# Kernel tuning notes

Hardware: AMD Instinct MI355X
Metric: run time of the kernel (lower is better)

## Reference

```python
import jax, jax.numpy as jnp
import numpy as np

# Static config (matches init_kwargs)
H, G, D = 16, 4, 128          # n_head, n_query_groups, head_size
QPK = H // G                  # queries per kv group = 4
LEFT = 1024 - 1               # sliding-window left width (local_window-1)
SCALE = 1.0 / float(np.sqrt(D))
NEG = jnp.finfo(jnp.float32).min


def _rope(x, cos, sin):
    # x: [B,T,h,D]; cos/sin: [T, D/2]; non-interleaved (flash-attn) convention
    d2 = cos.shape[-1]
    x1, x2 = x[..., :d2], x[..., d2:]
    c = cos[None, :, None, :]
    s = sin[None, :, None, :]
    return jnp.concatenate([x1 * c - x2 * s, x1 * s + x2 * c], axis=-1)


def setup_inputs() -> dict:
    key = jax.random.key(0)
    ks = jax.random.split(key, 4)
    B, T, C = 1, 2048, 2048
    x = jax.random.normal(ks[0], (B, T, C), jnp.float32)
    # real RoPE tables, base 10000
    pos = jnp.arange(T, dtype=jnp.float32)
    inv_freq = 1.0 / (10000.0 ** (jnp.arange(0, D, 2, dtype=jnp.float32) / D))
    ang = pos[:, None] * inv_freq[None, :]        # [T, D/2]
    cos, sin = jnp.cos(ang), jnp.sin(ang)
    W_attn = jax.random.normal(ks[1], ((H + 2 * G) * D, C), jnp.float32) * 0.02
    W_proj = jax.random.normal(ks[2], (C, H * D), jnp.float32) * 0.02
    k_sink = jax.random.normal(ks[3], (G * D,), jnp.float32) * 0.02
    v_sink = jnp.zeros((G * D,), jnp.float32)     # buffer, zeros in original
    return {"x": x, "cos": cos, "sin": sin, "W_attn": W_attn,
            "W_proj": W_proj, "k_sink": k_sink, "v_sink": v_sink}


def reference(x, cos, sin, W_attn, W_proj, k_sink, v_sink):
    B, T, C = x.shape
    # fused QKV projection (no bias)
    qkv = jnp.einsum('btc,oc->bto', x, W_attn)                 # [B,T,(H+2G)*D]
    qkv = qkv.reshape(B, T, G, QPK + 2, D)
    q = qkv[:, :, :, :QPK, :].reshape(B, T, H, D)              # [B,T,H,D]
    k = qkv[:, :, :, QPK, :]                                   # [B,T,G,D]
    v = qkv[:, :, :, QPK + 1, :]                               # [B,T,G,D]
    # RoPE on q and k
    q = _rope(q, cos, sin)
    k = _rope(k, cos, sin)
    # prepend sink token to k/v -> seqlen_k = T+1
    k = jnp.concatenate([jnp.broadcast_to(k_sink.reshape(1, 1, G, D), (B, 1, G, D)), k], axis=1)
    v = jnp.concatenate([jnp.broadcast_to(v_sink.reshape(1, 1, G, D), (B, 1, G, D)), v], axis=1)
    Tk = T + 1
    # GQA: group-major query head layout -> head h uses kv group h // QPK
    kh = jnp.repeat(k, QPK, axis=2)                            # [B,Tk,H,D]
    vh = jnp.repeat(v, QPK, axis=2)
    scores = jnp.einsum('bqhd,bkhd->bhqk', q, kh) * SCALE      # [B,H,T,Tk]
    # flash-attn causal + sliding window, bottom-right aligned: offset = Tk - T
    off = Tk - T
    i = jnp.arange(T)[:, None]
    j = jnp.arange(Tk)[None, :]
    allowed = (j <= i + off) & (j >= i + off - LEFT)
    scores = jnp.where(allowed[None, None], scores, NEG)
    p = jax.nn.softmax(scores, axis=-1)
    o = jnp.einsum('bhqk,bkhd->bqhd', p, vh).reshape(B, T, H * D)
    y = jnp.einsum('btd,cd->btc', o, W_proj)                   # output proj, no bias
    return y
```

## Files before the change

### kernel.cpp

```cpp
#include <hip/hip_runtime.h>

#define T_SEQ  2048
#define TK_SEQ 2049
#define JP     2080
#define SCALE_F 0.08838834764831845f
#define SL_F    0.12751744f
#define THR_L2  11.0f

typedef __attribute__((ext_vector_type(8))) short short8;
typedef __attribute__((ext_vector_type(4))) float f32x4;

__device__ __forceinline__ unsigned short f2bf(float f) {
  unsigned int u = __float_as_uint(f);
  u += 0x7fff + ((u >> 16) & 1);
  return (unsigned short)(u >> 16);
}

__global__ __launch_bounds__(256) void split_pack(const float4* __restrict__ s0,
                                                  uint4* __restrict__ d0, int n0,
                                                  const float4* __restrict__ s1,
                                                  uint4* __restrict__ d1, int n1) {
  int i = blockIdx.x * 256 + threadIdx.x;
  const float4* s; uint4* d; int k;
  if (i < n0) { s = s0; d = d0; k = i; }
  else { k = i - n0; if (k >= n1) return; s = s1; d = d1; }
  float4 f = s[k];
  unsigned int h0 = __float_as_uint(f.x) & 0xffff0000u;
  unsigned int h1 = __float_as_uint(f.y) & 0xffff0000u;
  unsigned int h2 = __float_as_uint(f.z) & 0xffff0000u;
  unsigned int h3 = __float_as_uint(f.w) & 0xffff0000u;
  unsigned int l0 = f2bf(f.x - __uint_as_float(h0));
  unsigned int l1 = f2bf(f.y - __uint_as_float(h1));
  unsigned int l2 = f2bf(f.z - __uint_as_float(h2));
  unsigned int l3 = f2bf(f.w - __uint_as_float(h3));
  uint4 o;
  o.x = (h0 >> 16) | (h1 & 0xffff0000u);
  o.y = (h2 >> 16) | (h3 & 0xffff0000u);
  o.z = l0 | (l1 << 16);
  o.w = l2 | (l3 << 16);
  d[k] = o;
}

#define LDK 56

__global__ __launch_bounds__(256, 3) void gemm_sp(const uint4* __restrict__ As,
                                                  const uint4* __restrict__ Bs,
                                                  float* __restrict__ C,
                                                  int M, int N, int K) {
  __shared__ unsigned short Ah[128 * LDK], Al[128 * LDK];
  __shared__ unsigned short Bh[64 * LDK],  Bl[64 * LDK];

  const int tid  = threadIdx.x;
  const int lane = tid & 63;
  const int wid  = tid >> 6;
  const int wm   = (wid >> 1) << 6;
  const int wn   = (wid & 1) << 5;
  const int lo16 = lane & 15;
  const int hi4  = lane >> 4;
  const int m0   = blockIdx.y << 7;
  const int n0   = blockIdx.x << 6;
  const int Kg   = K >> 2;

  const uint4* pa[4];
  const uint4* pb[2];
  int waofs[4], wbofs[2];
#pragma unroll
  for (int v = 0; v < 4; ++v) {
    int id = (v << 8) + tid;
    int r  = id >> 3;
    int kc = (id & 7) << 2;
    pa[v]    = As + (size_t)(m0 + r) * Kg + (kc >> 2);
    waofs[v] = r * LDK + kc;
  }
#pragma unroll
  for (int v = 0; v < 2; ++v) {
    int id = (v << 8) + tid;
    int r  = id >> 3;
    int kc = (id & 7) << 2;
    pb[v]    = Bs + (size_t)(n0 + r) * Kg + (kc >> 2);
    wbofs[v] = r * LDK + kc;
  }

  int ra[4], rb[2];
#pragma unroll
  for (int i = 0; i < 4; ++i) ra[i] = (wm + i * 16 + lo16) * LDK + (hi4 << 3);
#pragma unroll
  for (int j = 0; j < 2; ++j) rb[j] = (wn + j * 16 + lo16) * LDK + (hi4 << 3);

  f32x4 acc[4][2];
  const f32x4 z4 = {0.f, 0.f, 0.f, 0.f};
#pragma unroll
  for (int i = 0; i < 4; ++i)
#pragma unroll
    for (int j = 0; j < 2; ++j) acc[i][j] = z4;

  uint4 av[4], bv[2];
#pragma unroll
  for (int v = 0; v < 4; ++v) av[v] = pa[v][0];
#pragma unroll
  for (int v = 0; v < 2; ++v) bv[v] = pb[v][0];

  for (int k0 = 0; k0 < K; k0 += 32) {
    __syncthreads();
#pragma unroll
    for (int v = 0; v < 4; ++v) {
      uint2 ah = {av[v].x, av[v].y}, al = {av[v].z, av[v].w};
      *(uint2*)&Ah[waofs[v]] = ah;
      *(uint2*)&Al[waofs[v]] = al;
    }
#pragma unroll
    for (int v = 0; v < 2; ++v) {
      uint2 bh = {bv[v].x, bv[v].y}, bl = {bv[v].z, bv[v].w};
      *(uint2*)&Bh[wbofs[v]] = bh;
      *(uint2*)&Bl[wbofs[v]] = bl;
    }
    __syncthreads();
    if (k0 + 32 < K) {
      int kg = (k0 + 32) >> 2;
#pragma unroll
      for (int v = 0; v < 4; ++v) av[v] = pa[v][kg];
#pragma unroll
      for (int v = 0; v < 2; ++v) bv[v] = pb[v][kg];
    }
    short8 fah[4], fal[4], fbh[2], fbl[2];
#pragma unroll
    for (int i = 0; i < 4; ++i) {
      fah[i] = *(const short8*)&Ah[ra[i]];
      fal[i] = *(const short8*)&Al[ra[i]];
    }
#pragma unroll
    for (int j = 0; j < 2; ++j) {
      fbh[j] = *(const short8*)&Bh[rb[j]];
      fbl[j] = *(const short8*)&Bl[rb[j]];
    }
#pragma unroll
    for (int i = 0; i < 4; ++i)
#pragma unroll
      for (int j = 0; j < 2; ++j) {
        acc[i][j] = __builtin_amdgcn_mfma_f32_16x16x32_bf16(fah[i], fbh[j], acc[i][j], 0, 0, 0);
        acc[i][j] = __builtin_amdgcn_mfma_f32_16x16x32_bf16(fal[i], fbh[j], acc[i][j], 0, 0, 0);
        acc[i][j] = __builtin_amdgcn_mfma_f32_16x16x32_bf16(fah[i], fbl[j], acc[i][j], 0, 0, 0);
      }
  }

#pragma unroll
  for (int i = 0; i < 4; ++i) {
    const int row = m0 + wm + i * 16 + (hi4 << 2);
#pragma unroll
    for (int j = 0; j < 2; ++j) {
      float* cp = C + (size_t)row * N + n0 + wn + j * 16 + lo16;
      cp[0]            = acc[i][j][0];
      cp[(size_t)N]    = acc[i][j][1];
      cp[(size_t)2*N]  = acc[i][j][2];
      cp[(size_t)3*N]  = acc[i][j][3];
    }
  }
}

#define RB_Q  4096
#define RB_K  1024
#define RB_KE 64
#define RB_V  65

__global__ __launch_bounds__(256) void rope2(const float* __restrict__ qkv,
                                             const float* __restrict__ cosb,
                                             const float* __restrict__ sinb,
                                             const float* __restrict__ ksink,
                                             const float* __restrict__ vsink,
                                             unsigned short* __restrict__ qb,
                                             unsigned short* __restrict__ kb,
                                             unsigned short* __restrict__ vtb) {
  __shared__ unsigned short tl[512 * 33];
  const int bid = blockIdx.x, tid = threadIdx.x;
  if (bid < RB_Q) {
    int idx = bid * 256 + tid;
    int t = idx >> 9, rem = idx & 511;
    int h = rem >> 5, dp = (rem & 31) << 1;
    int g = h >> 2, qi = h & 3;
    const float* src = qkv + (size_t)t * 3072 + g * 768 + qi * 128;
    float2 x1 = *(const float2*)(src + dp);
    float2 x2 = *(const float2*)(src + 64 + dp);
    float2 c  = *(const float2*)(cosb + t * 64 + dp);
    float2 s  = *(const float2*)(sinb + t * 64 + dp);
    ushort2 o1 = { f2bf(x1.x * c.x - x2.x * s.x), f2bf(x1.y * c.y - x2.y * s.y) };
    ushort2 o2 = { f2bf(x1.x * s.x + x2.x * c.x), f2bf(x1.y * s.y + x2.y * c.y) };
    *(ushort2*)(qb + (size_t)t * 2048 + h * 128 + dp)      = o1;
    *(ushort2*)(qb + (size_t)t * 2048 + h * 128 + 64 + dp) = o2;
  } else if (bid < RB_Q + RB_K) {
    int idx = (bid - RB_Q) * 256 + tid;
    int t = idx >> 7, rem = idx & 127;
    int g = rem >> 5, dp = (rem & 31) << 1;
    const float* src = qkv + (size_t)t * 3072 + g * 768 + 512;
    float2 x1 = *(const float2*)(src + dp);
    float2 x2 = *(const float2*)(src + 64 + dp);
    float2 c  = *(const float2*)(cosb + t * 64 + dp);
    float2 s  = *(const float2*)(sinb + t * 64 + dp);
    ushort2 o1 = { f2bf(x1.x * c.x - x2.x * s.x), f2bf(x1.y * c.y - x2.y * s.y) };
    ushort2 o2 = { f2bf(x1.x * s.x + x2.x * c.x), f2bf(x1.y * s.y + x2.y * c.y) };
    size_t base = (size_t)(t + 1) * 512 + g * 128 + dp;
    *(ushort2*)(kb + base)      = o1;
    *(ushort2*)(kb + base + 64) = o2;
  } else if (bid < RB_Q + RB_K + RB_KE) {
    int idx = (bid - RB_Q - RB_K) * 256 + tid;
    int jj = idx >> 9, c = idx & 511;
    if (jj == 0) kb[c] = f2bf(ksink[c]);
    else         kb[(size_t)(2048 + jj) * 512 + c] = 0;
  } else {
    int b  = bid - RB_Q - RB_K - RB_KE;
    int j0 = b << 5;
#pragma unroll 4
    for (int st = 0; st < 64; ++st) {
      int id = st * 256 + tid;
      int jj = id >> 9, c = id & 511;
      int j = j0 + jj;
      float val;
      if (j == 0)          val = vsink[c];
      else if (j <= T_SEQ) val = qkv[(size_t)(j - 1) * 3072 + (c >> 7) * 768 + 640 + (c & 127)];
      else                 val = 0.f;
      tl[c * 33 + jj] = f2bf(val);
    }
    __syncthreads();
#pragma unroll 4
    for (int st = 0; st < 32; ++st) {
      int id = st * 256 + tid;
      int row = id >> 4, jp = (id & 15) << 1;
      ushort2 w = { tl[row * 33 + jp], tl[row * 33 + jp + 1] };
      *(ushort2*)(vtb + (size_t)row * JP + j0 + jp) = w;
    }
  }
}

#define KSTR 136
#define VSTR 40

__global__ __launch_bounds__(512) void attn_mfma_bf16(const unsigned short* __restrict__ qb,
                                                      const unsigned short* __restrict__ kb,
                                                      const unsigned short* __restrict__ vtb,
                                                      uint4* __restrict__ ofs) {
  __shared__ unsigned short Kl[2][32 * KSTR];
  __shared__ unsigned short Vl[2][128 * VSTR];

  const int bid  = blockIdx.x;
  const int tile = bid >> 2;
  const int g    = bid & 3;
  const int t0b  = tile << 5;
  const int tid  = threadIdx.x;
  const int wv   = tid >> 6;
  const int hq   = wv & 3;
  const int sub  = wv >> 2;
  const int h    = g * 4 + hq;
  const int lane = tid & 63;
  const int lo   = lane & 15;
  const int hi   = lane >> 4;
  const int t0w  = t0b + (sub << 4);
  const int t    = t0w + lo;

  const int sj   = tid >> 4;
  const int sc   = (tid & 15) << 3;
  const int kphi = ((((sj & 7) << 2) | (sj >> 3))) * KSTR + sc;
  const int svd  = tid >> 2;
  const int svj  = (tid & 3) << 3;
  const int vdst = svd * VSTR + svj;
  const unsigned short* ksrc = kb  + (size_t)sj * 512 + g * 128 + sc;
  const unsigned short* vsrc = vtb + (size_t)(g * 128 + svd) * JP + svj;

  short8 qfrag[4];
  {
    const unsigned short* qp = qb + (size_t)t * 2048 + h * 128 + (hi << 3);
#pragma unroll
    for (int d0 = 0; d0 < 4; ++d0) qfrag[d0] = *(const short8*)(qp + d0 * 32);
  }

  f32x4 acc[8];
  const f32x4 z4 = {0.f, 0.f, 0.f, 0.f};
#pragma unroll
  for (int dt = 0; dt < 8; ++dt) acc[dt] = z4;

  float m = -1e4f, l = 0.f;

  int jlo = t0b - 1022; if (jlo < 0) jlo = 0;
  const int jb0  = jlo & ~31;
  const int jmax = t0b + 32;
  const int nch  = ((jmax - jb0) >> 5) + 1;

  const int klA = (((lo & 3) << 2) | (lo >> 2)) * KSTR + (hi << 3);

  uint4 kreg = *(const uint4*)(ksrc + (size_t)jb0 * 512);
  uint4 vreg = *(const uint4*)(vsrc + jb0);
  *(uint4*)&Kl[0][kphi] = kreg;
  *(uint4*)&Vl[0][vdst] = vreg;
  __syncthreads();

  int bsel = 0;
  for (int ci = 0; ci < nch; ++ci) {
    const int jb = jb0 + (ci << 5);
    const bool more = (ci + 1 < nch);
    if (more) {
      const int jn = jb + 32;
      kreg = *(const uint4*)(ksrc + (size_t)jn * 512);
      vreg = *(const uint4*)(vsrc + jn);
    }

    const unsigned short* Kb = &Kl[bsel][0];
    f32x4 sa = z4, sb = z4;
#pragma unroll
    for (int d0 = 0; d0 < 4; ++d0) {
      short8 ka  = *(const short8*)(Kb + klA + d0 * 32);
      short8 kB2 = *(const short8*)(Kb + klA + 16 * KSTR + d0 * 32);
      sa = __builtin_amdgcn_mfma_f32_16x16x32_bf16(ka,  qfrag[d0], sa, 0, 0, 0);
      sb = __builtin_amdgcn_mfma_f32_16x16x32_bf16(kB2, qfrag[d0], sb, 0, 0, 0);
    }

    float z[8];
    const int jbase = jb + (hi << 3);
    const bool interior = (jb >= t0w - 1007) && (jb <= t0w - 30);
    if (interior) {
#pragma unroll
      for (int r = 0; r < 4; ++r) { z[r] = sa[r] * SL_F; z[r + 4] = sb[r] * SL_F; }
    } else {
#pragma unroll
      for (int r = 0; r < 8; ++r) {
        float sv = (r < 4) ? sa[r] : sb[r - 4];
        int j = jbase + r;
        bool valid = (j <= t + 1) && (j >= t - 1022);
        z[r] = valid ? sv * SL_F : -1e30f;
      }
    }

    float lmax = fmaxf(fmaxf(fmaxf(z[0], z[1]), fmaxf(z[2], z[3])),
                       fmaxf(fmaxf(z[4], z[5]), fmaxf(z[6], z[7])));
    if (!__all(lmax <= m + THR_L2)) {
      float cm = lmax;
      cm = fmaxf(cm, __shfl_xor(cm, 16, 64));
      cm = fmaxf(cm, __shfl_xor(cm, 32, 64));
      float mn = fmaxf(m, cm);
      float a  = exp2f(m - mn);
      l *= a;
#pragma unroll
      for (int dt = 0; dt < 8; ++dt) acc[dt] *= a;
      m = mn;
    }

    float p[8];
#pragma unroll
    for (int r = 0; r < 8; ++r) { p[r] = exp2f(z[r] - m); l += p[r]; }

    short8 pfrag;
#pragma unroll
    for (int e = 0; e < 8; ++e) pfrag[e] = (short)f2bf(p[e]);

    const unsigned short* Vb = &Vl[bsel][0];
#pragma unroll
    for (int dt = 0; dt < 8; ++dt) {
      short8 vf = *(const short8*)(Vb + (dt * 16 + lo) * VSTR + (hi << 3));
      acc[dt] = __builtin_amdgcn_mfma_f32_16x16x32_bf16(vf, pfrag, acc[dt], 0, 0, 0);
    }

    if (more) {
      *(uint4*)&Kl[bsel ^ 1][kphi] = kreg;
      *(uint4*)&Vl[bsel ^ 1][vdst] = vreg;
      __syncthreads();
      bsel ^= 1;
    }
  }

  float lt = l;
  lt += __shfl_xor(lt, 16, 64);
  lt += __shfl_xor(lt, 32, 64);
  const float inv = 1.f / lt;

  const size_t elem = (size_t)t * 2048 + h * 128 + (hi << 2);
#pragma unroll
  for (int dt = 0; dt < 8; ++dt) {
    f32x4 o4 = acc[dt] * inv;
    unsigned int h0 = __float_as_uint(o4[0]) & 0xffff0000u;
    unsigned int h1 = __float_as_uint(o4[1]) & 0xffff0000u;
    unsigned int h2 = __float_as_uint(o4[2]) & 0xffff0000u;
    unsigned int h3 = __float_as_uint(o4[3]) & 0xffff0000u;
    unsigned int l0 = f2bf(o4[0] - __uint_as_float(h0));
    unsigned int l1 = f2bf(o4[1] - __uint_as_float(h1));
    unsigned int l2 = f2bf(o4[2] - __uint_as_float(h2));
    unsigned int l3 = f2bf(o4[3] - __uint_as_float(h3));
    uint4 pk;
    pk.x = (h0 >> 16) | (h1 & 0xffff0000u);
    pk.y = (h2 >> 16) | (h3 & 0xffff0000u);
    pk.z = l0 | (l1 << 16);
    pk.w = l2 | (l3 << 16);
    ofs[(elem >> 2) + dt * 4] = pk;
  }
}

extern "C" void kernel_launch(void* const* d_in, const int* in_sizes, int n_in,
                              void* d_out, int out_size, void* d_ws, size_t ws_size,
                              hipStream_t stream) {
  const float* x     = (const float*)d_in[0];
  const float* cosb  = (const float*)d_in[1];
  const float* sinb  = (const float*)d_in[2];
  const float* Wa    = (const float*)d_in[3];
  const float* Wp    = (const float*)d_in[4];
  const float* ksink = (const float*)d_in[5];
  const float* vsink = (const float*)d_in[6];
  float* y = (float*)d_out;

  char* ws = (char*)d_ws;
  float*          qkv = (float*)ws;
  uint4*          wps = (uint4*)ws;
  uint4*          was = (uint4*)(ws + 25165824);
  uint4*          ofs = (uint4*)(ws + 25165824);
  uint4*          xs  = (uint4*)(ws + 50331648);
  unsigned short* qb  = (unsigned short*)(ws + 50331648);
  unsigned short* kbb = (unsigned short*)(ws + 58720256);
  unsigned short* vtb = (unsigned short*)(ws + 60850176);

  split_pack<<<10240, 256, 0, stream>>>((const float4*)x, xs, 1048576,
                                        (const float4*)Wa, was, 1572864);
  gemm_sp<<<dim3(48, 16), 256, 0, stream>>>(xs, was, qkv, 2048, 3072, 2048);
  rope2<<<RB_Q + RB_K + RB_KE + RB_V, 256, 0, stream>>>(qkv, cosb, sinb, ksink, vsink,
                                                        qb, kbb, vtb);
  split_pack<<<4096, 256, 0, stream>>>((const float4*)Wp, wps, 1048576,
                                       (const float4*)Wp, wps, 0);
  attn_mfma_bf16<<<256, 512, 0, stream>>>(qb, kbb, vtb, ofs);
  gemm_sp<<<dim3(32, 16), 256, 0, stream>>>(ofs, wps, y, 2048, 2048, 2048);
}
```

Before: 325.3 us.

## Store split bf16 hi/lo planes separately and load GEMM tiles directly into LDS

```diff
diff --git a/kernel.cpp b/kernel.cpp
--- a/kernel.cpp
+++ b/kernel.cpp
@@ -3,7 +3,6 @@
 #define T_SEQ  2048
 #define TK_SEQ 2049
 #define JP     2080
-#define SCALE_F 0.08838834764831845f
 #define SL_F    0.12751744f
 #define THR_L2  11.0f
 
@@ -16,39 +15,41 @@
   return (unsigned short)(u >> 16);
 }
 
+__device__ __forceinline__ void gload16(const unsigned short* g, unsigned short* l) {
+  __builtin_amdgcn_global_load_lds(
+      (const __attribute__((address_space(1))) void*)g,
+      (__attribute__((address_space(3))) void*)l, 16, 0, 0);
+}
+
 __global__ __launch_bounds__(256) void split_pack(const float4* __restrict__ s0,
-                                                  uint4* __restrict__ d0, int n0,
+                                                  unsigned short* __restrict__ d0,
+                                                  int n0, int p0,
                                                   const float4* __restrict__ s1,
-                                                  uint4* __restrict__ d1, int n1) {
+                                                  unsigned short* __restrict__ d1,
+                                                  int n1, int p1) {
   int i = blockIdx.x * 256 + threadIdx.x;
-  const float4* s; uint4* d; int k;
-  if (i < n0) { s = s0; d = d0; k = i; }
-  else { k = i - n0; if (k >= n1) return; s = s1; d = d1; }
+  const float4* s; unsigned short* d; int k, p;
+  if (i < n0) { s = s0; d = d0; k = i; p = p0; }
+  else { k = i - n0; if (k >= n1) return; s = s1; d = d1; p = p1; }
   float4 f = s[k];
-  unsigned int h0 = __float_as_uint(f.x) & 0xffff0000u;
-  unsigned int h1 = __float_as_uint(f.y) & 0xffff0000u;
-  unsigned int h2 = __float_as_uint(f.z) & 0xffff0000u;
-  unsigned int h3 = __float_as_uint(f.w) & 0xffff0000u;
-  unsigned int l0 = f2bf(f.x - __uint_as_float(h0));
-  unsigned int l1 = f2bf(f.y - __uint_as_float(h1));
-  unsigned int l2 = f2bf(f.z - __uint_as_float(h2));
-  unsigned int l3 = f2bf(f.w - __uint_as_float(h3));
-  uint4 o;
-  o.x = (h0 >> 16) | (h1 & 0xffff0000u);
-  o.y = (h2 >> 16) | (h3 & 0xffff0000u);
-  o.z = l0 | (l1 << 16);
-  o.w = l2 | (l3 << 16);
-  d[k] = o;
-}
-
-#define LDK 56
-
-__global__ __launch_bounds__(256, 3) void gemm_sp(const uint4* __restrict__ As,
-                                                  const uint4* __restrict__ Bs,
+  float fv[4] = {f.x, f.y, f.z, f.w};
+  ushort4 hv, lv;
+#pragma unroll
+  for (int e = 0; e < 4; ++e) {
+    unsigned int u = __float_as_uint(fv[e]) & 0xffff0000u;
+    ((unsigned short*)&hv)[e] = (unsigned short)(u >> 16);
+    ((unsigned short*)&lv)[e] = f2bf(fv[e] - __uint_as_float(u));
+  }
+  *(ushort4*)(d + 4 * (size_t)k)     = hv;
+  *(ushort4*)(d + p + 4 * (size_t)k) = lv;
+}
+
+__global__ __launch_bounds__(256, 3) void gemm_sp(const unsigned short* __restrict__ Ag,
+                                                  const unsigned short* __restrict__ Bg,
                                                   float* __restrict__ C,
                                                   int M, int N, int K) {
-  __shared__ unsigned short Ah[128 * LDK], Al[128 * LDK];
-  __shared__ unsigned short Bh[64 * LDK],  Bl[64 * LDK];
+  __shared__ unsigned short Ah[128 * 32], Al[128 * 32];
+  __shared__ unsigned short Bh[64 * 32],  Bl[64 * 32];
 
   const int tid  = threadIdx.x;
   const int lane = tid & 63;
@@ -59,33 +60,27 @@
   const int hi4  = lane >> 4;
   const int m0   = blockIdx.y << 7;
   const int n0   = blockIdx.x << 6;
-  const int Kg   = K >> 2;
-
-  const uint4* pa[4];
-  const uint4* pb[2];
-  int waofs[4], wbofs[2];
-#pragma unroll
-  for (int v = 0; v < 4; ++v) {
-    int id = (v << 8) + tid;
-    int r  = id >> 3;
-    int kc = (id & 7) << 2;
-    pa[v]    = As + (size_t)(m0 + r) * Kg + (kc >> 2);
-    waofs[v] = r * LDK + kc;
-  }
-#pragma unroll
-  for (int v = 0; v < 2; ++v) {
-    int id = (v << 8) + tid;
-    int r  = id >> 3;
-    int kc = (id & 7) << 2;
-    pb[v]    = Bs + (size_t)(n0 + r) * Kg + (kc >> 2);
-    wbofs[v] = r * LDK + kc;
-  }
+  const size_t MK = (size_t)M * K;
+  const size_t NK = (size_t)N * K;
+
+  const int ca0 = (wid << 6) + lane;
+  const int ca1 = ((4 + wid) << 6) + lane;
+  const int cb  = (wid << 6) + lane;
+  const unsigned short* a0g = Ag + (size_t)(m0 + (ca0 >> 2)) * K + ((ca0 & 3) << 3);
+  const unsigned short* a1g = Ag + (size_t)(m0 + (ca1 >> 2)) * K + ((ca1 & 3) << 3);
+  const unsigned short* bg  = Bg + (size_t)(n0 + (cb  >> 2)) * K + ((cb  & 3) << 3);
+  unsigned short* a0d  = &Ah[wid << 9];
+  unsigned short* a1d  = &Ah[(4 + wid) << 9];
+  unsigned short* al0d = &Al[wid << 9];
+  unsigned short* al1d = &Al[(4 + wid) << 9];
+  unsigned short* bhd  = &Bh[wid << 9];
+  unsigned short* bld  = &Bl[wid << 9];
 
   int ra[4], rb[2];
 #pragma unroll
-  for (int i = 0; i < 4; ++i) ra[i] = (wm + i * 16 + lo16) * LDK + (hi4 << 3);
-#pragma unroll
-  for (int j = 0; j < 2; ++j) rb[j] = (wn + j * 16 + lo16) * LDK + (hi4 << 3);
+  for (int i = 0; i < 4; ++i) ra[i] = ((wm + i * 16 + lo16) << 5) + (hi4 << 3);
+#pragma unroll
+  for (int j = 0; j < 2; ++j) rb[j] = ((wn + j * 16 + lo16) << 5) + (hi4 << 3);
 
   f32x4 acc[4][2];
   const f32x4 z4 = {0.f, 0.f, 0.f, 0.f};
@@ -94,34 +89,16 @@
 #pragma unroll
     for (int j = 0; j < 2; ++j) acc[i][j] = z4;
 
-  uint4 av[4], bv[2];
-#pragma unroll
-  for (int v = 0; v < 4; ++v) av[v] = pa[v][0];
-#pragma unroll
-  for (int v = 0; v < 2; ++v) bv[v] = pb[v][0];
-
   for (int k0 = 0; k0 < K; k0 += 32) {
     __syncthreads();
-#pragma unroll
-    for (int v = 0; v < 4; ++v) {
-      uint2 ah = {av[v].x, av[v].y}, al = {av[v].z, av[v].w};
-      *(uint2*)&Ah[waofs[v]] = ah;
-      *(uint2*)&Al[waofs[v]] = al;
-    }
-#pragma unroll
-    for (int v = 0; v < 2; ++v) {
-      uint2 bh = {bv[v].x, bv[v].y}, bl = {bv[v].z, bv[v].w};
-      *(uint2*)&Bh[wbofs[v]] = bh;
-      *(uint2*)&Bl[wbofs[v]] = bl;
-    }
+    gload16(a0g + k0, a0d);
+    gload16(a1g + k0, a1d);
+    gload16(a0g + MK + k0, al0d);
+    gload16(a1g + MK + k0, al1d);
+    gload16(bg + k0, bhd);
+    gload16(bg + NK + k0, bld);
     __syncthreads();
-    if (k0 + 32 < K) {
-      int kg = (k0 + 32) >> 2;
-#pragma unroll
-      for (int v = 0; v < 4; ++v) av[v] = pa[v][kg];
-#pragma unroll
-      for (int v = 0; v < 2; ++v) bv[v] = pb[v][kg];
-    }
+
     short8 fah[4], fal[4], fbh[2], fbl[2];
 #pragma unroll
     for (int i = 0; i < 4; ++i) {
@@ -236,7 +213,7 @@
 __global__ __launch_bounds__(512) void attn_mfma_bf16(const unsigned short* __restrict__ qb,
                                                       const unsigned short* __restrict__ kb,
                                                       const unsigned short* __restrict__ vtb,
-                                                      uint4* __restrict__ ofs) {
+                                                      unsigned short* __restrict__ ofh) {
   __shared__ unsigned short Kl[2][32 * KSTR];
   __shared__ unsigned short Vl[2][128 * VSTR];
 
@@ -369,24 +346,20 @@
   lt += __shfl_xor(lt, 32, 64);
   const float inv = 1.f / lt;
 
+  unsigned short* ofl = ofh + 4194304;
   const size_t elem = (size_t)t * 2048 + h * 128 + (hi << 2);
 #pragma unroll
   for (int dt = 0; dt < 8; ++dt) {
     f32x4 o4 = acc[dt] * inv;
-    unsigned int h0 = __float_as_uint(o4[0]) & 0xffff0000u;
-    unsigned int h1 = __float_as_uint(o4[1]) & 0xffff0000u;
-    unsigned int h2 = __float_as_uint(o4[2]) & 0xffff0000u;
-    unsigned int h3 = __float_as_uint(o4[3]) & 0xffff0000u;
-    unsigned int l0 = f2bf(o4[0] - __uint_as_float(h0));
-    unsigned int l1 = f2bf(o4[1] - __uint_as_float(h1));
-    unsigned int l2 = f2bf(o4[2] - __uint_as_float(h2));
-    unsigned int l3 = f2bf(o4[3] - __uint_as_float(h3));
-    uint4 pk;
-    pk.x = (h0 >> 16) | (h1 & 0xffff0000u);
-    pk.y = (h2 >> 16) | (h3 & 0xffff0000u);
-    pk.z = l0 | (l1 << 16);
-    pk.w = l2 | (l3 << 16);
-    ofs[(elem >> 2) + dt * 4] = pk;
+    ushort4 hv, lv;
+#pragma unroll
+    for (int e = 0; e < 4; ++e) {
+      unsigned int u = __float_as_uint(o4[e]) & 0xffff0000u;
+      ((unsigned short*)&hv)[e] = (unsigned short)(u >> 16);
+      ((unsigned short*)&lv)[e] = f2bf(o4[e] - __uint_as_float(u));
+    }
+    *(ushort4*)(ofh + elem + dt * 16) = hv;
+    *(ushort4*)(ofl + elem + dt * 16) = lv;
   }
 }
 
@@ -404,21 +377,21 @@
 
   char* ws = (char*)d_ws;
   float*          qkv = (float*)ws;
-  uint4*          wps = (uint4*)ws;
-  uint4*          was = (uint4*)(ws + 25165824);
-  uint4*          ofs = (uint4*)(ws + 25165824);
-  uint4*          xs  = (uint4*)(ws + 50331648);
+  unsigned short* wps = (unsigned short*)ws;
+  unsigned short* was = (unsigned short*)(ws + 25165824);
+  unsigned short* ofh = (unsigned short*)(ws + 25165824);
+  unsigned short* xs  = (unsigned short*)(ws + 50331648);
   unsigned short* qb  = (unsigned short*)(ws + 50331648);
   unsigned short* kbb = (unsigned short*)(ws + 58720256);
   unsigned short* vtb = (unsigned short*)(ws + 60850176);
 
-  split_pack<<<10240, 256, 0, stream>>>((const float4*)x, xs, 1048576,
-                                        (const float4*)Wa, was, 1572864);
+  split_pack<<<10240, 256, 0, stream>>>((const float4*)x, xs, 1048576, 4194304,
+                                        (const float4*)Wa, was, 1572864, 6291456);
   gemm_sp<<<dim3(48, 16), 256, 0, stream>>>(xs, was, qkv, 2048, 3072, 2048);
   rope2<<<RB_Q + RB_K + RB_KE + RB_V, 256, 0, stream>>>(qkv, cosb, sinb, ksink, vsink,
                                                         qb, kbb, vtb);
-  split_pack<<<4096, 256, 0, stream>>>((const float4*)Wp, wps, 1048576,
-                                       (const float4*)Wp, wps, 0);
-  attn_mfma_bf16<<<256, 512, 0, stream>>>(qb, kbb, vtb, ofs);
-  gemm_sp<<<dim3(32, 16), 256, 0, stream>>>(ofs, wps, y, 2048, 2048, 2048);
-}
+  split_pack<<<4096, 256, 0, stream>>>((const float4*)Wp, wps, 1048576, 4194304,
+                                       (const float4*)Wp, wps, 0, 0);
+  attn_mfma_bf16<<<256, 512, 0, stream>>>(qb, kbb, vtb, ofh);
+  gemm_sp<<<dim3(32, 16), 256, 0, stream>>>(ofh, wps, y, 2048, 2048, 2048);
+}
```

After: 342.7 us. 5.3% more time.
